# Kernel optimization log

Hardware: AMD Instinct MI355X
Metric: run time of the kernel (lower is better)

The kernel has to match this reference:

```python
import jax, jax.numpy as jnp
import numpy as np

B, T, C, H = 2, 2048, 512, 8
HD = C // H  # head size = 64

def _layernorm(x, g, b, eps=1e-5):
    mu = jnp.mean(x, axis=-1, keepdims=True)
    var = jnp.var(x, axis=-1, keepdims=True)
    return (x - mu) * jax.lax.rsqrt(var + eps) * g + b

def setup_inputs() -> dict:
    key = jax.random.key(0)
    ks = jax.random.split(key, 12)
    s_attn = 1.0 / np.sqrt(C)
    s_proj = 1.0 / np.sqrt(H * HD)
    s_ffn1 = 1.0 / np.sqrt(C)
    s_ffn2 = 1.0 / np.sqrt(4 * C)
    return {
        "x":   jax.random.normal(ks[0], (B, T, C), jnp.float32),
        "Wq":  jax.random.uniform(ks[1], (H, C, HD), jnp.float32, -s_attn, s_attn),
        "Wk":  jax.random.uniform(ks[2], (H, C, HD), jnp.float32, -s_attn, s_attn),
        "Wv":  jax.random.uniform(ks[3], (H, C, HD), jnp.float32, -s_attn, s_attn),
        "Wo":  jax.random.uniform(ks[4], (H * HD, C), jnp.float32, -s_proj, s_proj),
        "bo":  jax.random.uniform(ks[5], (C,), jnp.float32, -s_proj, s_proj),
        "W1":  jax.random.uniform(ks[6], (C, 4 * C), jnp.float32, -s_ffn1, s_ffn1),
        "b1":  jax.random.uniform(ks[7], (4 * C,), jnp.float32, -s_ffn1, s_ffn1),
        "W2":  jax.random.uniform(ks[8], (4 * C, C), jnp.float32, -s_ffn2, s_ffn2),
        "b2":  jax.random.uniform(ks[9], (C,), jnp.float32, -s_ffn2, s_ffn2),
        "g1":  jnp.ones((C,), jnp.float32),
        "be1": jnp.zeros((C,), jnp.float32),
        "g2":  jnp.ones((C,), jnp.float32),
        "be2": jnp.zeros((C,), jnp.float32),
    }

def reference(x, Wq, Wk, Wv, Wo, bo, W1, b1, W2, b2, g1, be1, g2, be2):
    # --- multi-head causal self-attention on ln1(x) ---
    h = _layernorm(x, g1, be1)
    q = jnp.einsum("btc,hcd->bhtd", h, Wq)
    k = jnp.einsum("btc,hcd->bhtd", h, Wk)
    v = jnp.einsum("btc,hcd->bhtd", h, Wv)
    scores = jnp.einsum("bhtd,bhsd->bhts", q, k) * (HD ** -0.5)
    causal = jnp.tril(jnp.ones((T, T), bool))
    scores = jnp.where(causal, scores, -jnp.inf)
    wei = jax.nn.softmax(scores, axis=-1)
    attn = jnp.einsum("bhts,bhsd->bhtd", wei, v)
    attn = attn.transpose(0, 2, 1, 3).reshape(B, T, H * HD)  # concat heads
    x = x + attn @ Wo + bo
    # --- GELU MLP on ln2(x) ---
    h2 = _layernorm(x, g2, be2)
    ff = jax.nn.gelu(h2 @ W1 + b1, approximate=False) @ W2 + b2
    return x + ff
```

## Files before the change

### kernel.cpp

```cpp
#include <hip/hip_runtime.h>
#include <math.h>

constexpr int B_   = 2;
constexpr int T_   = 2048;
constexpr int C_   = 512;
constexpr int H_   = 8;
constexpr int HD_  = 64;
constexpr int M_   = B_ * T_;
constexpr int FF_  = 4 * C_;
constexpr int NQKV_ = 3 * C_;

typedef __attribute__((ext_vector_type(8))) short short8;
typedef __attribute__((ext_vector_type(4))) short short4v;
typedef __attribute__((ext_vector_type(4))) float floatx4;

static __device__ __forceinline__ unsigned short f2bf(float f) {
    union { float f; unsigned u; } v; v.f = f;
    unsigned r = v.u + 0x7fff + ((v.u >> 16) & 1);
    return (unsigned short)(r >> 16);
}

static __device__ __forceinline__ float bf2f(unsigned short s) {
    union { unsigned u; float f; } v; v.u = (unsigned)s << 16; return v.f;
}

static __device__ __forceinline__ unsigned packbf2(float a, float b) {
    union { float f; unsigned u; } x, y; x.f = a; y.f = b;
    unsigned lo = (x.u + 0x7fff + ((x.u >> 16) & 1)) >> 16;
    unsigned hi = (y.u + 0x7fff + ((y.u >> 16) & 1)) & 0xffff0000u;
    return lo | hi;
}

static __device__ __forceinline__ void gl2lds16(const unsigned short* g,
                                                unsigned short* l) {
    __builtin_amdgcn_global_load_lds(
        (const __attribute__((address_space(1))) void*)g,
        (__attribute__((address_space(3))) void*)l, 16, 0, 0);
}

#if __has_builtin(__builtin_amdgcn_mfma_f32_16x16x16bf16_1k)
static __device__ __forceinline__ floatx4 mfma16(short4v a, short4v b, floatx4 c) {
    return __builtin_amdgcn_mfma_f32_16x16x16bf16_1k(a, b, c, 0, 0, 0);
}
#elif __has_builtin(__builtin_amdgcn_mfma_f32_16x16x16_bf16)
static __device__ __forceinline__ floatx4 mfma16(short4v a, short4v b, floatx4 c) {
    return __builtin_amdgcn_mfma_f32_16x16x16_bf16(a, b, c, 0, 0, 0);
}
#else
static __device__ __forceinline__ floatx4 mfma16(short4v a, short4v b, floatx4 c) {
    asm volatile("v_mfma_f32_16x16x16_bf16 %0, %1, %2, %0"
                 : "+v"(c) : "v"(a), "v"(b));
    return c;
}
#endif

static __device__ __forceinline__ void ln_row(int row, int lane,
                                              const float* __restrict__ x,
                                              const float* __restrict__ g,
                                              const float* __restrict__ b,
                                              unsigned short* __restrict__ out) {
    const float* xr = x + (size_t)row * C_;
    int c0 = lane * 8;
    float4 v0 = *(const float4*)(xr + c0);
    float4 v1 = *(const float4*)(xr + c0 + 4);
    float vals[8] = {v0.x, v0.y, v0.z, v0.w, v1.x, v1.y, v1.z, v1.w};

    float s = 0.f, ss = 0.f;
#pragma unroll
    for (int j = 0; j < 8; j++) { s += vals[j]; ss += vals[j] * vals[j]; }
#pragma unroll
    for (int off = 32; off; off >>= 1) {
        s  += __shfl_xor(s,  off);
        ss += __shfl_xor(ss, off);
    }
    float mu  = s / C_;
    float var = ss / C_ - mu * mu;
    float rs  = rsqrtf(var + 1e-5f);

    unsigned short* orow = out + (size_t)row * C_;
#pragma unroll
    for (int j = 0; j < 8; j++) {
        int c = c0 + j;
        orow[c] = f2bf((vals[j] - mu) * rs * g[c] + b[c]);
    }
}

__global__ __launch_bounds__(256) void prologue(
        const float* __restrict__ Wq, const float* __restrict__ Wk,
        const float* __restrict__ Wv, const float* __restrict__ Wo,
        const float* __restrict__ W1, const float* __restrict__ W2,
        const float* __restrict__ x,  const float* __restrict__ g1,
        const float* __restrict__ be1,
        unsigned short* __restrict__ Wqkv_t, unsigned short* __restrict__ Wo_t,
        unsigned short* __restrict__ W1_t,   unsigned short* __restrict__ W2_t,
        unsigned short* __restrict__ hb) {
    int idx = blockIdx.x;
    int tid = threadIdx.x;
    if (idx >= 3072) {
        int row = (idx - 3072) * 4 + (tid >> 6);
        ln_row(row, tid & 63, x, g1, be1, hb);
        return;
    }
    __shared__ float tile[32][33];
    const float* src; unsigned short* dst;
    int K, N, k0, n0;
    float scale = 1.0f;
    if (idx < 768) {
        int wz = idx >> 8, rem = idx & 255;
        int h = rem >> 5, r2 = rem & 31;
        k0 = (r2 >> 1) * 32; n0 = (r2 & 1) * 32;
        src = (wz == 0 ? Wq : (wz == 1 ? Wk : Wv)) + (size_t)h * C_ * HD_;
        dst = Wqkv_t + (size_t)(wz * C_ + h * HD_) * C_;
        K = C_; N = HD_;
        if (wz == 0) scale = 0.125f;
    } else if (idx < 1024) {
        int rem = idx - 768;
        n0 = (rem & 15) * 32; k0 = (rem >> 4) * 32;
        src = Wo; dst = Wo_t; K = C_; N = C_;
    } else if (idx < 2048) {
        int rem = idx - 1024;
        n0 = (rem & 63) * 32; k0 = (rem >> 6) * 32;
        src = W1; dst = W1_t; K = C_; N = FF_;
    } else {
        int rem = idx - 2048;
        n0 = (rem & 15) * 32; k0 = (rem >> 4) * 32;
        src = W2; dst = W2_t; K = FF_; N = C_;
    }
    int tx = tid & 31, ty = tid >> 5;
#pragma unroll
    for (int i = 0; i < 4; i++)
        tile[ty + i * 8][tx] = src[(size_t)(k0 + ty + i * 8) * N + n0 + tx];
    __syncthreads();
#pragma unroll
    for (int i = 0; i < 4; i++)
        dst[(size_t)(n0 + ty + i * 8) * K + k0 + tx] = f2bf(tile[tx][ty + i * 8] * scale);
}

__global__ __launch_bounds__(256) void ln_kernel(
        const float* __restrict__ x, const float* __restrict__ g,
        const float* __restrict__ b, unsigned short* __restrict__ out) {
    int tid = threadIdx.x;
    int row = blockIdx.x * 4 + (tid >> 6);
    ln_row(row, tid & 63, x, g, b, out);
}

template<int BM, int BN, int BK>
__global__ __launch_bounds__(256) void mfma_gemm(
        const unsigned short* __restrict__ A,
        const unsigned short* __restrict__ Bt,
        const float* __restrict__ bias,
        const float* __restrict__ resid,
        float* __restrict__ outF,
        unsigned short* __restrict__ outB,
        unsigned short* __restrict__ vT,
        int M, int N, int K, int flags) {
    constexpr int WM = BM / 2, WN = BN / 2;
    constexpr int MI = WM / 16, NI = WN / 16, KH = BK / 32;
    __shared__ unsigned short smem[KH * (BM + BN) * 32];
    unsigned short* As = smem;
    unsigned short* Bs = smem + KH * BM * 32;

    int t = threadIdx.x;
    int lane = t & 63, w = t >> 6;
    int wr = (w >> 1) * WM, wc = (w & 1) * WN;
    int lm = lane & 15, lq = lane >> 4;
    int m0 = blockIdx.y * BM, n0 = blockIdx.x * BN;

    floatx4 acc[MI][NI];
#pragma unroll
    for (int mi = 0; mi < MI; mi++)
#pragma unroll
        for (int ni = 0; ni < NI; ni++) acc[mi][ni] = (floatx4){0.f, 0.f, 0.f, 0.f};

    for (int k0 = 0; k0 < K; k0 += BK) {
        __syncthreads();
#pragma unroll
        for (int hh = 0; hh < KH; hh++) {
#pragma unroll
            for (int j = 0; j < BM * 4 / 256; j++) {
                int i = t + j * 256;
                gl2lds16(A + (size_t)(m0 + (i >> 2)) * K + k0 + hh * 32 + (i & 3) * 8,
                         &As[hh * BM * 32 + i * 8]);
            }
#pragma unroll
            for (int j = 0; j < BN * 4 / 256; j++) {
                int i = t + j * 256;
                gl2lds16(Bt + (size_t)(n0 + (i >> 2)) * K + k0 + hh * 32 + (i & 3) * 8,
                         &Bs[hh * BN * 32 + i * 8]);
            }
        }
        __syncthreads();

#pragma unroll
        for (int hh = 0; hh < KH; hh++) {
            short8 af[MI], bfv[NI];
#pragma unroll
            for (int mi = 0; mi < MI; mi++)
                af[mi] = *(const short8*)&As[hh * BM * 32 + (wr + mi * 16 + lm) * 32 + lq * 8];
#pragma unroll
            for (int ni = 0; ni < NI; ni++)
                bfv[ni] = *(const short8*)&Bs[hh * BN * 32 + (wc + ni * 16 + lm) * 32 + lq * 8];
#pragma unroll
            for (int mi = 0; mi < MI; mi++)
#pragma unroll
                for (int ni = 0; ni < NI; ni++)
                    acc[mi][ni] = __builtin_amdgcn_mfma_f32_16x16x32_bf16(
                        af[mi], bfv[ni], acc[mi][ni], 0, 0, 0);
        }
    }

    if ((flags & 16) && n0 >= 2 * C_) {
        __syncthreads();
        unsigned short* Ts = smem;
#pragma unroll
        for (int mi = 0; mi < MI; mi++)
#pragma unroll
            for (int ni = 0; ni < NI; ni++) {
                int cl = wc + ni * 16 + lm;
#pragma unroll
                for (int r = 0; r < 4; r++)
                    Ts[cl * 72 + wr + mi * 16 + lq * 4 + r] = f2bf(acc[mi][ni][r]);
            }
        __syncthreads();
        int b = m0 >> 11, trow = m0 & (T_ - 1);
#pragma unroll
        for (int it = 0; it < BN * (BM / 8) / 256; it++) {
            int u = it * 256 + t;
            int cl = u >> 3, seg = u & 7;
            int vcol = n0 - 2 * C_ + cl;
            int hh2 = vcol >> 6, dd = vcol & 63;
            short8 vv = *(const short8*)&Ts[cl * 72 + seg * 8];
            *(short8*)&vT[(size_t)((b * H_ + hh2) * HD_ + dd) * T_ + trow + seg * 8] = vv;
        }
        return;
    }

#pragma unroll
    for (int mi = 0; mi < MI; mi++)
#pragma unroll
        for (int ni = 0; ni < NI; ni++) {
            int gc = n0 + wc + ni * 16 + lm;
#pragma unroll
            for (int r = 0; r < 4; r++) {
                int gr = m0 + wr + mi * 16 + lq * 4 + r;
                float v = acc[mi][ni][r];
                if (flags & 1) v += bias[gc];
                if (flags & 4) v = 0.5f * v * (1.0f + erff(v * 0.70710678118654752f));
                if (flags & 2) v += resid[(size_t)gr * N + gc];
                if (flags & 8) outB[(size_t)gr * N + gc] = f2bf(v);
                else           outF[(size_t)gr * N + gc] = v;
            }
        }
}

__global__ __launch_bounds__(256, 4) void attn_mfma(
        const unsigned short* __restrict__ qkv,
        const unsigned short* __restrict__ vT,
        unsigned short* __restrict__ oP,
        float* __restrict__ lP) {
    __shared__ unsigned short Ks[2][64 * 72];
    __shared__ unsigned short Vt[2][64 * 72];

    int t = threadIdx.x;
    int wq = t >> 6, lane = t & 63;
    int lm = lane & 15, quad = lane >> 4;
    int bh = blockIdx.y, b = bh >> 3, h = bh & 7;
    int tile = blockIdx.x >> 1, s = blockIdx.x & 1;
    int q0 = tile * 64;

    int srow = t >> 2, sq4 = t & 3;

    const unsigned short* kbase = qkv + (size_t)(b * T_) * NQKV_ + C_ + h * HD_;
    const unsigned short* vbase = vT + (size_t)(bh * HD_ + srow) * T_;

    int gq_row = q0 + wq * 16 + lm;
    const unsigned short* qp = qkv + (size_t)(b * T_ + gq_row) * NQKV_ + h * HD_;
    short8 qf0 = *(const short8*)(qp + quad * 8);
    short8 qf1 = *(const short8*)(qp + 32 + quad * 8);

    float l_s = 0.f;
    floatx4 o_acc[4];
#pragma unroll
    for (int dt = 0; dt < 4; dt++) o_acc[dt] = (floatx4){0.f, 0.f, 0.f, 0.f};

    short8 kp0, kp1, vp0, vp1;
    if (s <= tile) {
        int s0 = s * 64;
        const unsigned short* kg = kbase + (size_t)(s0 + srow) * NQKV_ + sq4 * 16;
        kp0 = *(const short8*)kg;
        kp1 = *(const short8*)(kg + 8);
        vp0 = *(const short8*)(vbase + s0 + sq4 * 16);
        vp1 = *(const short8*)(vbase + s0 + sq4 * 16 + 8);
        *(short8*)&Ks[0][srow * 72 + sq4 * 16]     = kp0;
        *(short8*)&Ks[0][srow * 72 + sq4 * 16 + 8] = kp1;
        *(short8*)&Vt[0][srow * 72 + sq4 * 16]     = vp0;
        *(short8*)&Vt[0][srow * 72 + sq4 * 16 + 8] = vp1;
    }

    int buf = 0;
    for (int c = s; c <= tile; c += 2) {
        bool havenext = (c + 2 <= tile);
        if (havenext) {
            int s0n = (c + 2) * 64;
            const unsigned short* kgn = kbase + (size_t)(s0n + srow) * NQKV_ + sq4 * 16;
            kp0 = *(const short8*)kgn;
            kp1 = *(const short8*)(kgn + 8);
            vp0 = *(const short8*)(vbase + s0n + sq4 * 16);
            vp1 = *(const short8*)(vbase + s0n + sq4 * 16 + 8);
        }
        __syncthreads();

        bool diag = (c == tile);
#pragma unroll
        for (int kt = 0; kt < 4; kt++) {
            if (diag && kt > wq) continue;
            short8 kf0 = *(const short8*)&Ks[buf][(kt * 16 + lm) * 72 + quad * 8];
            short8 kf1 = *(const short8*)&Ks[buf][(kt * 16 + lm) * 72 + 32 + quad * 8];
            floatx4 sv = (floatx4){0.f, 0.f, 0.f, 0.f};
            sv = __builtin_amdgcn_mfma_f32_16x16x32_bf16(kf0, qf0, sv, 0, 0, 0);
            sv = __builtin_amdgcn_mfma_f32_16x16x32_bf16(kf1, qf1, sv, 0, 0, 0);
            float p0, p1, p2, p3;
            {
                bool e = diag && (kt == wq);
                p0 = (e && (quad * 4 + 0 > lm)) ? 0.f : __expf(sv[0]);
                p1 = (e && (quad * 4 + 1 > lm)) ? 0.f : __expf(sv[1]);
                p2 = (e && (quad * 4 + 2 > lm)) ? 0.f : __expf(sv[2]);
                p3 = (e && (quad * 4 + 3 > lm)) ? 0.f : __expf(sv[3]);
            }
            l_s += (p0 + p1) + (p2 + p3);
            uint2 pu;
            pu.x = packbf2(p0, p1);
            pu.y = packbf2(p2, p3);
            short4v pk = *(short4v*)&pu;
#pragma unroll
            for (int dt = 0; dt < 4; dt++) {
                short4v vf = *(const short4v*)&Vt[buf][(dt * 16 + lm) * 72 + kt * 16 + quad * 4];
                o_acc[dt] = mfma16(pk, vf, o_acc[dt]);
            }
        }
        if (havenext) {
            int nb = buf ^ 1;
            *(short8*)&Ks[nb][srow * 72 + sq4 * 16]     = kp0;
            *(short8*)&Ks[nb][srow * 72 + sq4 * 16 + 8] = kp1;
            *(short8*)&Vt[nb][srow * 72 + sq4 * 16]     = vp0;
            *(short8*)&Vt[nb][srow * 72 + sq4 * 16 + 8] = vp1;
        }
        buf ^= 1;
    }

    float lsum = l_s;
    lsum += __shfl_xor(lsum, 16);
    lsum += __shfl_xor(lsum, 32);
    if (quad == 0)
        lP[(size_t)s * M_ * H_ + (size_t)(b * T_ + q0 + wq * 16 + lm) * H_ + h] = lsum;
    unsigned short* obase = oP + (size_t)s * M_ * C_;
#pragma unroll
    for (int r = 0; r < 4; r++) {
        int gq = q0 + wq * 16 + quad * 4 + r;
        unsigned short* op = obase + (size_t)(b * T_ + gq) * C_ + h * HD_ + lm;
#pragma unroll
        for (int dt = 0; dt < 4; dt++)
            op[dt * 16] = f2bf(o_acc[dt][r]);
    }
}

__global__ __launch_bounds__(256) void attn_combine(
        const unsigned short* __restrict__ oP,
        const float* __restrict__ lP,
        unsigned short* __restrict__ o) {
    int row = blockIdx.x * 4 + (threadIdx.x >> 6);
    int lane = threadIdx.x & 63;
    int h = lane >> 3;
    float l0 = lP[(size_t)row * H_ + h];
    float l1 = lP[(size_t)M_ * H_ + (size_t)row * H_ + h];
    float inv = 1.f / (l0 + l1);
    int c0 = lane * 8;
    const unsigned short* p0 = oP + (size_t)row * C_ + c0;
    const unsigned short* p1 = oP + (size_t)M_ * C_ + (size_t)row * C_ + c0;
    unsigned short* op = o + (size_t)row * C_ + c0;
    short8 a = *(const short8*)p0;
    short8 b = *(const short8*)p1;
#pragma unroll
    for (int j = 0; j < 8; j++)
        op[j] = f2bf((bf2f((unsigned short)a[j]) + bf2f((unsigned short)b[j])) * inv);
}

extern "C" void kernel_launch(void* const* d_in, const int* in_sizes, int n_in,
                              void* d_out, int out_size, void* d_ws, size_t ws_size,
                              hipStream_t stream) {
    const float* x   = (const float*)d_in[0];
    const float* Wq  = (const float*)d_in[1];
    const float* Wk  = (const float*)d_in[2];
    const float* Wv  = (const float*)d_in[3];
    const float* Wo  = (const float*)d_in[4];
    const float* bo  = (const float*)d_in[5];
    const float* W1  = (const float*)d_in[6];
    const float* b1  = (const float*)d_in[7];
    const float* W2  = (const float*)d_in[8];
    const float* b2  = (const float*)d_in[9];
    const float* g1  = (const float*)d_in[10];
    const float* be1 = (const float*)d_in[11];
    const float* g2  = (const float*)d_in[12];
    const float* be2 = (const float*)d_in[13];
    float* out = (float*)d_out;

    unsigned short* Wqkv_t = (unsigned short*)d_ws;
    unsigned short* Wo_t   = Wqkv_t + (size_t)NQKV_ * C_;
    unsigned short* W1_t   = Wo_t   + (size_t)C_ * C_;
    unsigned short* W2_t   = W1_t   + (size_t)C_ * FF_;
    unsigned short* hb     = W2_t   + (size_t)FF_ * C_;
    unsigned short* attnb  = hb     + (size_t)M_ * C_;
    unsigned short* qkvb   = attnb  + (size_t)M_ * C_;
    unsigned short* vTb    = qkvb   + (size_t)M_ * NQKV_;
    unsigned short* oPb    = vTb    + (size_t)M_ * C_;
    float*          lPf    = (float*)(oPb + 2 * (size_t)M_ * C_);
    unsigned short* ff1    = attnb;

    prologue<<<4096, 256, 0, stream>>>(Wq, Wk, Wv, Wo, W1, W2, x, g1, be1,
                                       Wqkv_t, Wo_t, W1_t, W2_t, hb);

    mfma_gemm<64, 128, 64><<<dim3(NQKV_ / 128, M_ / 64), 256, 0, stream>>>(
        hb, Wqkv_t, nullptr, nullptr, nullptr, qkvb, vTb, M_, NQKV_, C_, 8 | 16);

    attn_mfma<<<dim3(64, B_ * H_), 256, 0, stream>>>(qkvb, vTb, oPb, lPf);

    attn_combine<<<M_ / 4, 256, 0, stream>>>(oPb, lPf, attnb);

    mfma_gemm<64, 64, 64><<<dim3(C_ / 64, M_ / 64), 256, 0, stream>>>(
        attnb, Wo_t, bo, x, out, nullptr, nullptr, M_, C_, C_, 1 | 2);

    ln_kernel<<<M_ / 4, 256, 0, stream>>>(out, g2, be2, hb);

    mfma_gemm<64, 128, 64><<<dim3(FF_ / 128, M_ / 64), 256, 0, stream>>>(
        hb, W1_t, b1, nullptr, nullptr, ff1, nullptr, M_, FF_, C_, 1 | 4 | 8);

    mfma_gemm<64, 64, 64><<<dim3(C_ / 64, M_ / 64), 256, 0, stream>>>(
        ff1, W2_t, b2, out, out, nullptr, nullptr, M_, C_, FF_, 1 | 2);
}
```

Baseline: 219.2 us.

## Fuse attention combine into Wo GEMM, split-K W2 with atomics, bigger FFN tiles

Removes the separate attention-combine kernel by merging the two partial attention outputs and their normalisation inside the Wo GEMM's A-tile load, which replaces the async global-to-LDS copy with register loads. The second LayerNorm kernel now also writes x+b2 back into the output, so the W2 GEMM can run split-K over 4 z-slices and atomically accumulate into out without its own bias or residual epilogue. The FFN GEMMs move to 128x128 tiles. This trades a launch and an intermediate round trip for float atomics, which make the sums non-deterministic, and for a slower synchronous A load in the Wo GEMM.

Measured after the change: 233.8 us. +6.7%, slower.

```diff
diff --git a/kernel.cpp b/kernel.cpp
--- a/kernel.cpp
+++ b/kernel.cpp
@@ -58,7 +58,9 @@
                                               const float* __restrict__ x,
                                               const float* __restrict__ g,
                                               const float* __restrict__ b,
-                                              unsigned short* __restrict__ out) {
+                                              unsigned short* __restrict__ out,
+                                              const float* __restrict__ badd,
+                                              float* __restrict__ xmut) {
     const float* xr = x + (size_t)row * C_;
     int c0 = lane * 8;
     float4 v0 = *(const float4*)(xr + c0);
@@ -82,6 +84,16 @@
     for (int j = 0; j < 8; j++) {
         int c = c0 + j;
         orow[c] = f2bf((vals[j] - mu) * rs * g[c] + b[c]);
+    }
+    if (badd) {
+        float* xw = xmut + (size_t)row * C_;
+        float4 w0, w1;
+        w0.x = vals[0] + badd[c0];     w0.y = vals[1] + badd[c0 + 1];
+        w0.z = vals[2] + badd[c0 + 2]; w0.w = vals[3] + badd[c0 + 3];
+        w1.x = vals[4] + badd[c0 + 4]; w1.y = vals[5] + badd[c0 + 5];
+        w1.z = vals[6] + badd[c0 + 6]; w1.w = vals[7] + badd[c0 + 7];
+        *(float4*)(xw + c0)     = w0;
+        *(float4*)(xw + c0 + 4) = w1;
     }
 }
 
@@ -98,7 +110,7 @@
     int tid = threadIdx.x;
     if (idx >= 3072) {
         int row = (idx - 3072) * 4 + (tid >> 6);
-        ln_row(row, tid & 63, x, g1, be1, hb);
+        ln_row(row, tid & 63, x, g1, be1, hb, nullptr, nullptr);
         return;
     }
     __shared__ float tile[32][33];
@@ -138,10 +150,11 @@
 
 __global__ __launch_bounds__(256) void ln_kernel(
         const float* __restrict__ x, const float* __restrict__ g,
-        const float* __restrict__ b, unsigned short* __restrict__ out) {
+        const float* __restrict__ b, unsigned short* __restrict__ out,
+        const float* __restrict__ badd, float* __restrict__ xmut) {
     int tid = threadIdx.x;
     int row = blockIdx.x * 4 + (tid >> 6);
-    ln_row(row, tid & 63, x, g, b, out);
+    ln_row(row, tid & 63, x, g, b, out, badd, xmut);
 }
 
 template<int BM, int BN, int BK>
@@ -153,6 +166,7 @@
         float* __restrict__ outF,
         unsigned short* __restrict__ outB,
         unsigned short* __restrict__ vT,
+        const float* __restrict__ lP,
         int M, int N, int K, int flags) {
     constexpr int WM = BM / 2, WN = BN / 2;
     constexpr int MI = WM / 16, NI = WN / 16, KH = BK / 32;
@@ -165,6 +179,8 @@
     int wr = (w >> 1) * WM, wc = (w & 1) * WN;
     int lm = lane & 15, lq = lane >> 4;
     int m0 = blockIdx.y * BM, n0 = blockIdx.x * BN;
+    int kper = K / gridDim.z;
+    int kbeg = blockIdx.z * kper, kend = kbeg + kper;
 
     floatx4 acc[MI][NI];
 #pragma unroll
@@ -172,23 +188,52 @@
 #pragma unroll
         for (int ni = 0; ni < NI; ni++) acc[mi][ni] = (floatx4){0.f, 0.f, 0.f, 0.f};
 
-    for (int k0 = 0; k0 < K; k0 += BK) {
+    for (int k0 = kbeg; k0 < kend; k0 += BK) {
         __syncthreads();
-#pragma unroll
-        for (int hh = 0; hh < KH; hh++) {
-#pragma unroll
-            for (int j = 0; j < BM * 4 / 256; j++) {
-                int i = t + j * 256;
-                gl2lds16(A + (size_t)(m0 + (i >> 2)) * K + k0 + hh * 32 + (i & 3) * 8,
-                         &As[hh * BM * 32 + i * 8]);
-            }
+        if (flags & 32) {
+#pragma unroll
+            for (int hh = 0; hh < KH; hh++) {
+#pragma unroll
+                for (int j = 0; j < BM * 4 / 256; j++) {
+                    int i = t + j * 256;
+                    int gr = m0 + (i >> 2);
+                    int f = k0 + hh * 32 + (i & 3) * 8;
+                    const unsigned short* pa = A + (size_t)gr * K + f;
+                    short8 a8 = *(const short8*)pa;
+                    short8 b8 = *(const short8*)(pa + (size_t)M_ * C_);
+                    float l0 = lP[(size_t)gr * H_ + (f >> 6)];
+                    float l1 = lP[(size_t)(M_ + gr) * H_ + (f >> 6)];
+                    float inv = 1.f / (l0 + l1);
+                    unsigned pk[4];
+#pragma unroll
+                    for (int q = 0; q < 4; q++) {
+                        float v0 = (bf2f((unsigned short)a8[2 * q]) +
+                                    bf2f((unsigned short)b8[2 * q])) * inv;
+                        float v1 = (bf2f((unsigned short)a8[2 * q + 1]) +
+                                    bf2f((unsigned short)b8[2 * q + 1])) * inv;
+                        pk[q] = packbf2(v0, v1);
+                    }
+                    *(short8*)&As[hh * BM * 32 + i * 8] = *(short8*)pk;
+                }
+            }
+        } else {
+#pragma unroll
+            for (int hh = 0; hh < KH; hh++)
+#pragma unroll
+                for (int j = 0; j < BM * 4 / 256; j++) {
+                    int i = t + j * 256;
+                    gl2lds16(A + (size_t)(m0 + (i >> 2)) * K + k0 + hh * 32 + (i & 3) * 8,
+                             &As[hh * BM * 32 + i * 8]);
+                }
+        }
+#pragma unroll
+        for (int hh = 0; hh < KH; hh++)
 #pragma unroll
             for (int j = 0; j < BN * 4 / 256; j++) {
                 int i = t + j * 256;
                 gl2lds16(Bt + (size_t)(n0 + (i >> 2)) * K + k0 + hh * 32 + (i & 3) * 8,
                          &Bs[hh * BN * 32 + i * 8]);
             }
-        }
         __syncthreads();
 
 #pragma unroll
@@ -232,6 +277,21 @@
             short8 vv = *(const short8*)&Ts[cl * 72 + seg * 8];
             *(short8*)&vT[(size_t)((b * H_ + hh2) * HD_ + dd) * T_ + trow + seg * 8] = vv;
         }
+        return;
+    }
+
+    if (flags & 64) {
+#pragma unroll
+        for (int mi = 0; mi < MI; mi++)
+#pragma unroll
+            for (int ni = 0; ni < NI; ni++) {
+                int gc = n0 + wc + ni * 16 + lm;
+#pragma unroll
+                for (int r = 0; r < 4; r++) {
+                    int gr = m0 + wr + mi * 16 + lq * 4 + r;
+                    atomicAdd(&outF[(size_t)gr * N + gc], acc[mi][ni][r]);
+                }
+            }
         return;
     }
 
@@ -362,27 +422,6 @@
         for (int dt = 0; dt < 4; dt++)
             op[dt * 16] = f2bf(o_acc[dt][r]);
     }
-}
-
-__global__ __launch_bounds__(256) void attn_combine(
-        const unsigned short* __restrict__ oP,
-        const float* __restrict__ lP,
-        unsigned short* __restrict__ o) {
-    int row = blockIdx.x * 4 + (threadIdx.x >> 6);
-    int lane = threadIdx.x & 63;
-    int h = lane >> 3;
-    float l0 = lP[(size_t)row * H_ + h];
-    float l1 = lP[(size_t)M_ * H_ + (size_t)row * H_ + h];
-    float inv = 1.f / (l0 + l1);
-    int c0 = lane * 8;
-    const unsigned short* p0 = oP + (size_t)row * C_ + c0;
-    const unsigned short* p1 = oP + (size_t)M_ * C_ + (size_t)row * C_ + c0;
-    unsigned short* op = o + (size_t)row * C_ + c0;
-    short8 a = *(const short8*)p0;
-    short8 b = *(const short8*)p1;
-#pragma unroll
-    for (int j = 0; j < 8; j++)
-        op[j] = f2bf((bf2f((unsigned short)a[j]) + bf2f((unsigned short)b[j])) * inv);
 }
 
 extern "C" void kernel_launch(void* const* d_in, const int* in_sizes, int n_in,
@@ -420,20 +459,21 @@
                                        Wqkv_t, Wo_t, W1_t, W2_t, hb);
 
     mfma_gemm<64, 128, 64><<<dim3(NQKV_ / 128, M_ / 64), 256, 0, stream>>>(
-        hb, Wqkv_t, nullptr, nullptr, nullptr, qkvb, vTb, M_, NQKV_, C_, 8 | 16);
+        hb, Wqkv_t, nullptr, nullptr, nullptr, qkvb, vTb, nullptr,
+        M_, NQKV_, C_, 8 | 16);
 
     attn_mfma<<<dim3(64, B_ * H_), 256, 0, stream>>>(qkvb, vTb, oPb, lPf);
 
-    attn_combine<<<M_ / 4, 256, 0, stream>>>(oPb, lPf, attnb);
-
     mfma_gemm<64, 64, 64><<<dim3(C_ / 64, M_ / 64), 256, 0, stream>>>(
-        attnb, Wo_t, bo, x, out, nullptr, nullptr, M_, C_, C_, 1 | 2);
-
-    ln_kernel<<<M_ / 4, 256, 0, stream>>>(out, g2, be2, hb);
-
-    mfma_gemm<64, 128, 64><<<dim3(FF_ / 128, M_ / 64), 256, 0, stream>>>(
-        hb, W1_t, b1, nullptr, nullptr, ff1, nullptr, M_, FF_, C_, 1 | 4 | 8);
-
-    mfma_gemm<64, 64, 64><<<dim3(C_ / 64, M_ / 64), 256, 0, stream>>>(
-        ff1, W2_t, b2, out, out, nullptr, nullptr, M_, C_, FF_, 1 | 2);
-}
+        oPb, Wo_t, bo, x, out, nullptr, nullptr, lPf, M_, C_, C_, 1 | 2 | 32);
+
+    ln_kernel<<<M_ / 4, 256, 0, stream>>>(out, g2, be2, hb, b2, out);
+
+    mfma_gemm<128, 128, 64><<<dim3(FF_ / 128, M_ / 128), 256, 0, stream>>>(
+        hb, W1_t, b1, nullptr, nullptr, ff1, nullptr, nullptr,
+        M_, FF_, C_, 1 | 4 | 8);
+
+    mfma_gemm<128, 128, 64><<<dim3(C_ / 128, M_ / 128, 4), 256, 0, stream>>>(
+        ff1, W2_t, nullptr, nullptr, out, nullptr, nullptr, nullptr,
+        M_, C_, FF_, 64);
+}
```
